# Kernel optimization log

Hardware: AMD Instinct MI355X
Metric: run time of the kernel (lower is better)

The kernel has to match this reference:

```python
import jax, jax.numpy as jnp
import numpy as np

N, E, H, L, B = 200000, 800000, 128, 4, 2000  # nodes, directed edges, hidden, layers, graphs
ATOM, BOND = 28, 6


def setup_inputs() -> dict:
    key = jax.random.key(0)
    ks = jax.random.split(key, 12)
    h = jax.random.normal(ks[0], (N, ATOM), jnp.float32)
    e = jax.random.normal(ks[1], (E, BOND), jnp.float32)
    # paired directed edges: edge 2i = (u->v), edge 2i+1 = (v->u), so rev(k) = k ^ 1
    u = jax.random.randint(ks[2], (E // 2,), 0, N)
    v = jax.random.randint(ks[3], (E // 2,), 0, N)
    src = jnp.stack([u, v], axis=1).reshape(-1)
    dst = jnp.stack([v, u], axis=1).reshape(-1)
    graph_id = jnp.sort(jax.random.randint(ks[4], (N,), 0, B))
    s = 1.0 / np.sqrt(H).astype(np.float32)
    W_emb = jax.random.normal(ks[5], (ATOM, H), jnp.float32) * (1.0 / np.sqrt(ATOM))
    W_init = jax.random.normal(ks[6], (H + BOND, H), jnp.float32) * s
    b_init = jnp.zeros((H,), jnp.float32)
    W_layers = jax.random.normal(ks[7], (L, H, H), jnp.float32) * s
    b_layers = jnp.zeros((L, H), jnp.float32)
    W_ro = jax.random.normal(ks[8], (H, H), jnp.float32) * s
    W_pred = jax.random.normal(ks[9], (H, 1), jnp.float32) * s
    b_pred = jnp.zeros((1,), jnp.float32)
    snorm_n = jnp.ones((N, 1), jnp.float32)
    snorm_e = jnp.ones((E, 1), jnp.float32)
    return dict(h=h, e=e, W_emb=W_emb, W_init=W_init, b_init=b_init,
                W_layers=W_layers, b_layers=b_layers, W_ro=W_ro,
                W_pred=W_pred, b_pred=b_pred, src=src, dst=dst,
                graph_id=graph_id, snorm_n=snorm_n, snorm_e=snorm_e)


def reference(h, e, W_emb, W_init, b_init, W_layers, b_layers, W_ro,
              W_pred, b_pred, src, dst, graph_id, snorm_n, snorm_e):
    n_nodes = h.shape[0]
    n_edges = src.shape[0]
    rev = jnp.arange(n_edges) ^ 1  # paired reverse-edge index
    # node embedding (dropout is identity at p=0); x kept as residual input per source
    x = h @ W_emb  # [N, H]
    # init_message_func: per-edge relu(Linear(cat(h_src, e)))
    he = jax.nn.relu(jnp.concatenate([x[src], e], axis=1) @ W_init + b_init)  # [E, H]
    # D-MPNN layers: aggregate incoming edge states at src node, exclude reverse edge,
    # linear + relu (norms disabled in this config), outer residual add
    n_layers = W_layers.shape[0]
    for l in range(n_layers):
        agg = jax.ops.segment_sum(he, dst, num_segments=n_nodes)  # sum of edge states into each node
        m = agg[src] - he[rev]                                    # exclude reverse edge
        he = jax.nn.relu(m @ W_layers[l] + b_layers[l]) + he      # residual
    # update_all(copy_edge, sum): node state = sum of incoming edge states
    h_out = jax.ops.segment_sum(he, dst, num_segments=n_nodes)  # [N, H]
    h_ro = h_out @ W_ro                                          # linear_ro (no bias)
    # readout == 'sum': per-graph sum of node states
    hg = jax.ops.segment_sum(h_ro, graph_id, num_segments=B)     # [B, H]
    return hg @ W_pred + b_pred                                  # [B, 1]
```

## Files before the change

kernel.cpp:

```cpp
#include <hip/hip_runtime.h>
#include <hip/hip_bf16.h>

#define H 128
#define ATOM 28
#define BOND 6
#define NLAYERS 4
#define TE 32
#define LW 136
#define LKI 72
typedef unsigned short US;
typedef unsigned int UI;
typedef short bf16x8 __attribute__((ext_vector_type(8)));
typedef float f32x4 __attribute__((ext_vector_type(4)));
#define MFMA(a,b,c) __builtin_amdgcn_mfma_f32_16x16x32_bf16((a),(b),(c),0,0,0)

__device__ __forceinline__ float bf2f(US u) {
    union { unsigned int i; float f; } v; v.i = ((unsigned int)u) << 16; return v.f;
}
__device__ __forceinline__ US f2bf(float f) {
    union { float f; unsigned int i; } v; v.f = f;
    unsigned int r = v.i + 0x7FFF + ((v.i >> 16) & 1);
    return (US)(r >> 16);
}
__device__ __forceinline__ float in_ld(const void* p, long long i, int bf) {
    return bf ? bf2f(((const US*)p)[i]) : ((const float*)p)[i];
}

__global__ void detect_kernel(const void* snorm, int* flag) {
    const US* u = (const US*)snorm;
    *flag = (u[0] == 0x3F80 && u[2] == 0x3F80) ? 1 : 0;
}

__global__ void fail_kernel(void* out, int nB, float val, const int* flag) {
    int i = blockIdx.x * 256 + threadIdx.x;
    if (i < nB) {
        if (*flag) ((US*)out)[i] = f2bf(val);
        else       ((float*)out)[i] = val;
    }
}

__global__ void build_wt(const void* __restrict__ W_emb, const void* __restrict__ W_init,
                         const int* __restrict__ flag, US* __restrict__ WtG) {
    int bf = *flag;
    int k = blockIdx.x;
    int c = threadIdx.x;
    float v = 0.f;
    if (k < ATOM) {
        for (int j = 0; j < H; ++j)
            v += in_ld(W_emb, k * H + j, bf) * in_ld(W_init, (long long)j * H + c, bf);
    } else if (k < ATOM + BOND) {
        v = in_ld(W_init, (long long)(H + k - ATOM) * H + c, bf);
    }
    WtG[c * 64 + k] = f2bf(v);
}

__global__ void build_wtL(const void* __restrict__ W_layers, const int* __restrict__ flag,
                          US* __restrict__ WtL) {
    int bf = *flag;
    int l = blockIdx.x >> 7, n = blockIdx.x & 127;
    int k = threadIdx.x;
    long long si = (long long)l * H * H + (long long)k * H + n;
    WtL[((long long)l * H + n) * H + k] = bf ? ((const US*)W_layers)[si]
                                             : f2bf(((const float*)W_layers)[si]);
}

__global__ void build_wtR(const void* __restrict__ W_ro, const int* __restrict__ flag,
                          US* __restrict__ WtR) {
    int bf = *flag;
    int n = blockIdx.x, k = threadIdx.x;
    long long si = (long long)k * H + n;
    WtR[(long long)n * H + k] = bf ? ((const US*)W_ro)[si]
                                   : f2bf(((const float*)W_ro)[si]);
}

__global__ void hist_kernel(const int* __restrict__ dst, int* __restrict__ cnt, int nE) {
    int k = blockIdx.x * 256 + threadIdx.x;
    if (k < nE) atomicAdd(&cnt[dst[k]], 1);
}

__global__ __launch_bounds__(256) void scan1(const int* __restrict__ cnt,
                                             int* __restrict__ rowptr,
                                             int* __restrict__ partials, int nN) {
    __shared__ int sd[256];
    int t = threadIdx.x;
    int base = blockIdx.x * 1024 + t * 4;
    int l0 = (base + 0 < nN) ? cnt[base + 0] : 0;
    int l1 = (base + 1 < nN) ? cnt[base + 1] : 0;
    int l2 = (base + 2 < nN) ? cnt[base + 2] : 0;
    int l3 = (base + 3 < nN) ? cnt[base + 3] : 0;
    int s = l0 + l1 + l2 + l3;
    sd[t] = s; __syncthreads();
    for (int off = 1; off < 256; off <<= 1) {
        int v = (t >= off) ? sd[t - off] : 0;
        __syncthreads();
        sd[t] += v;
        __syncthreads();
    }
    int excl = sd[t] - s;
    if (base + 0 < nN) rowptr[base + 0] = excl;
    if (base + 1 < nN) rowptr[base + 1] = excl + l0;
    if (base + 2 < nN) rowptr[base + 2] = excl + l0 + l1;
    if (base + 3 < nN) rowptr[base + 3] = excl + l0 + l1 + l2;
    if (t == 255) partials[blockIdx.x] = sd[255];
}

__global__ __launch_bounds__(256) void scan2(const int* __restrict__ partials,
                                             int* __restrict__ blockoff, int SB) {
    __shared__ int sd[256];
    int t = threadIdx.x;
    int v = (t < SB) ? partials[t] : 0;
    sd[t] = v; __syncthreads();
    for (int off = 1; off < 256; off <<= 1) {
        int x = (t >= off) ? sd[t - off] : 0;
        __syncthreads();
        sd[t] += x;
        __syncthreads();
    }
    blockoff[t] = sd[t] - v;
}

__global__ void scan3(int* __restrict__ rowptr, int* __restrict__ cursor,
                      const int* __restrict__ blockoff, int nN, int nE) {
    int i = blockIdx.x * 256 + threadIdx.x;
    if (i < nN) {
        int v = rowptr[i] + blockoff[i >> 10];
        rowptr[i] = v;
        cursor[i] = v;
    }
    if (i == 0) rowptr[nN] = nE;
}

__global__ void fill_kernel(const int* __restrict__ dst, int* __restrict__ cursor,
                            int* __restrict__ ein, int nE) {
    int k = blockIdx.x * 256 + threadIdx.x;
    if (k < nE) {
        int pos = atomicAdd(&cursor[dst[k]], 1);
        ein[pos] = k;
    }
}

__global__ __launch_bounds__(256) void agg_gather(
    const US* __restrict__ he, const int* __restrict__ rowptr,
    const int* __restrict__ ein, US* __restrict__ agg, int nN) {
    int n = blockIdx.x * 4 + (threadIdx.x >> 6);
    int lane = threadIdx.x & 63;
    if (n >= nN) return;
    const UI* heU = (const UI*)he;
    int s = rowptr[n], epos = rowptr[n + 1];
    float f0 = 0.f, f1 = 0.f;
    int idx = s;
    for (; idx + 4 <= epos; idx += 4) {
        int e0 = ein[idx], e1 = ein[idx + 1], e2 = ein[idx + 2], e3 = ein[idx + 3];
        UI u0 = heU[(long long)e0 * 64 + lane];
        UI u1 = heU[(long long)e1 * 64 + lane];
        UI u2 = heU[(long long)e2 * 64 + lane];
        UI u3 = heU[(long long)e3 * 64 + lane];
        f0 += bf2f((US)(u0 & 0xFFFF)) + bf2f((US)(u1 & 0xFFFF))
            + bf2f((US)(u2 & 0xFFFF)) + bf2f((US)(u3 & 0xFFFF));
        f1 += bf2f((US)(u0 >> 16)) + bf2f((US)(u1 >> 16))
            + bf2f((US)(u2 >> 16)) + bf2f((US)(u3 >> 16));
    }
    for (; idx < epos; ++idx) {
        UI u = heU[(long long)ein[idx] * 64 + lane];
        f0 += bf2f((US)(u & 0xFFFF));
        f1 += bf2f((US)(u >> 16));
    }
    ((UI*)agg)[(long long)n * 64 + lane] = (UI)f2bf(f0) | ((UI)f2bf(f1) << 16);
}

__global__ __launch_bounds__(256) void scatter_cas(
    const US* __restrict__ he, const int* __restrict__ dst,
    US* __restrict__ agg, long long totalPairs) {
    const UI* heU = (const UI*)he;
    UI* aggU = (UI*)agg;
    long long i = (long long)blockIdx.x * blockDim.x + threadIdx.x;
    long long stride = (long long)gridDim.x * blockDim.x;
    for (; i < totalPairs; i += stride) {
        int k = (int)(i >> 6);
        int jp = (int)(i & 63);
        UI pv = heU[i];
        float v0 = bf2f((US)(pv & 0xFFFF));
        float v1 = bf2f((US)(pv >> 16));
        UI* addr = aggU + (long long)dst[k] * 64 + jp;
        UI old = *addr, assumed;
        do {
            assumed = old;
            UI nv = (UI)f2bf(bf2f((US)(assumed & 0xFFFF)) + v0)
                  | ((UI)f2bf(bf2f((US)(assumed >> 16)) + v1) << 16);
            old = atomicCAS(addr, assumed, nv);
        } while (old != assumed);
    }
}

__global__ __launch_bounds__(256) void mfma_init(
    const void* __restrict__ h, const void* __restrict__ e,
    const US* __restrict__ WtG, const void* __restrict__ b_init,
    const int* __restrict__ src, const int* __restrict__ flag,
    US* __restrict__ he, int nE) {
    __shared__ __align__(16) US sA[TE * LKI];
    const int bf = *flag;
    const int tid = threadIdx.x;
    const int wave = tid >> 6, lane = tid & 63;
    const int quad = lane >> 4, l16 = lane & 15;
    const int ncol0 = wave * 32;
    float rb0 = in_ld(b_init, ncol0 + l16, bf);
    float rb1 = in_ld(b_init, ncol0 + 16 + l16, bf);
    bf16x8 bw[2][2];
    #pragma unroll
    for (int i = 0; i < 2; ++i)
        #pragma unroll
        for (int c = 0; c < 2; ++c)
            bw[i][c] = *(const bf16x8*)&WtG[(ncol0 + c * 16 + l16) * 64 + i * 32 + quad * 8];

    const int r = tid >> 3, u0 = (tid & 7) * 4;
    int ntiles = nE / TE;
    for (int t = blockIdx.x; t < ntiles; t += gridDim.x) {
        int k0 = t * TE;
        __syncthreads();
        {
            int k = k0 + r;
            int s = src[k];
            UI* dU = (UI*)&sA[r * LKI];
            if (bf) {
                const UI* hU = (const UI*)h;
                const UI* eU = (const UI*)e;
                #pragma unroll
                for (int q = 0; q < 4; ++q) {
                    int idx = u0 + q;
                    UI v = 0;
                    if (idx < 14) v = hU[(long long)s * 14 + idx];
                    else if (idx < 17) v = eU[(long long)k * 3 + (idx - 14)];
                    dU[idx] = v;
                }
            } else {
                const float* hF = (const float*)h;
                const float* eF = (const float*)e;
                #pragma unroll
                for (int q = 0; q < 4; ++q) {
                    int idx = u0 + q;
                    int c0 = idx * 2, c1 = idx * 2 + 1;
                    float f0 = 0.f, f1 = 0.f;
                    if (c0 < ATOM) f0 = hF[(long long)s * ATOM + c0];
                    else if (c0 < ATOM + BOND) f0 = eF[(long long)k * BOND + (c0 - ATOM)];
                    if (c1 < ATOM) f1 = hF[(long long)s * ATOM + c1];
                    else if (c1 < ATOM + BOND) f1 = eF[(long long)k * BOND + (c1 - ATOM)];
                    dU[idx] = (UI)f2bf(f0) | ((UI)f2bf(f1) << 16);
                }
            }
        }
        __syncthreads();

        f32x4 acc00 = {0,0,0,0}, acc01 = {0,0,0,0}, acc10 = {0,0,0,0}, acc11 = {0,0,0,0};
        #pragma unroll
        for (int i = 0; i < 2; ++i) {
            int kb = i * 32 + quad * 8;
            bf16x8 a0 = *(const bf16x8*)&sA[l16 * LKI + kb];
            bf16x8 a1 = *(const bf16x8*)&sA[(l16 + 16) * LKI + kb];
            acc00 = MFMA(a0, bw[i][0], acc00);
            acc01 = MFMA(a0, bw[i][1], acc01);
            acc10 = MFMA(a1, bw[i][0], acc10);
            acc11 = MFMA(a1, bw[i][1], acc11);
        }
        #pragma unroll
        for (int mt = 0; mt < 2; ++mt)
            #pragma unroll
            for (int reg = 0; reg < 4; ++reg) {
                int row = mt * 16 + quad * 4 + reg;
                long long hbase = (long long)(k0 + row) * H;
                #pragma unroll
                for (int nt = 0; nt < 2; ++nt) {
                    float a = mt ? (nt ? acc11[reg] : acc10[reg])
                                 : (nt ? acc01[reg] : acc00[reg]);
                    int col = ncol0 + nt * 16 + l16;
                    he[hbase + col] = f2bf(fmaxf(a + (nt ? rb1 : rb0), 0.f));
                }
            }
    }
}

__global__ __launch_bounds__(256) void mfma_layer(
    const US* __restrict__ agg, const int* __restrict__ src,
    const US* __restrict__ WtL, const void* __restrict__ b_layers,
    int layer, const int* __restrict__ flag, US* __restrict__ he, int nE) {
    __shared__ __align__(16) US sHe[TE * LW];
    __shared__ __align__(16) US sAgg[TE * LW];
    const int bf = *flag;
    const int tid = threadIdx.x;
    const int wave = tid >> 6, lane = tid & 63;
    const int quad = lane >> 4, l16 = lane & 15;
    const int ncol0 = wave * 32;
    float rb0 = in_ld(b_layers, (long long)layer * H + ncol0 + l16, bf);
    float rb1 = in_ld(b_layers, (long long)layer * H + ncol0 + 16 + l16, bf);
    const US* Wl = WtL + (size_t)layer * H * H;
    bf16x8 bw[4][2];
    #pragma unroll
    for (int i = 0; i < 4; ++i)
        #pragma unroll
        for (int c = 0; c < 2; ++c)
            bw[i][c] = *(const bf16x8*)&Wl[(ncol0 + c * 16 + l16) * H + i * 32 + quad * 8];

    int ntiles = nE / TE;
    for (int t = blockIdx.x; t < ntiles; t += gridDim.x) {
        int k0 = t * TE;
        __syncthreads();
        const uint4* heG = (const uint4*)(he + (long long)k0 * H);
        #pragma unroll
        for (int ii = 0; ii < 2; ++ii) {
            int i = tid + ii * 256;
            int r = i >> 4, q = i & 15;
            *(uint4*)&sHe[r * LW + q * 8] = heG[i];
            int s = src[k0 + r];
            *(uint4*)&sAgg[r * LW + q * 8] = ((const uint4*)(agg + (long long)s * H))[q];
        }
        __syncthreads();

        f32x4 g1a = {0,0,0,0}, g1b = {0,0,0,0}, g1c = {0,0,0,0}, g1d = {0,0,0,0};
        f32x4 g2a = {0,0,0,0}, g2b = {0,0,0,0}, g2c = {0,0,0,0}, g2d = {0,0,0,0};
        #pragma unroll
        for (int i = 0; i < 4; ++i) {
            int kb = i * 32 + quad * 8;
            bf16x8 aA0 = *(const bf16x8*)&sAgg[l16 * LW + kb];
            bf16x8 aA1 = *(const bf16x8*)&sAgg[(l16 + 16) * LW + kb];
            bf16x8 aH0 = *(const bf16x8*)&sHe[l16 * LW + kb];
            bf16x8 aH1 = *(const bf16x8*)&sHe[(l16 + 16) * LW + kb];
            g1a = MFMA(aA0, bw[i][0], g1a); g1b = MFMA(aA0, bw[i][1], g1b);
            g1c = MFMA(aA1, bw[i][0], g1c); g1d = MFMA(aA1, bw[i][1], g1d);
            g2a = MFMA(aH0, bw[i][0], g2a); g2b = MFMA(aH0, bw[i][1], g2b);
            g2c = MFMA(aH1, bw[i][0], g2c); g2d = MFMA(aH1, bw[i][1], g2d);
        }
        __syncthreads();

        #pragma unroll
        for (int mt = 0; mt < 2; ++mt)
            #pragma unroll
            for (int reg = 0; reg < 4; ++reg) {
                int row = mt * 16 + quad * 4 + reg;
                #pragma unroll
                for (int nt = 0; nt < 2; ++nt) {
                    float g1 = mt ? (nt ? g1d[reg] : g1c[reg])
                                  : (nt ? g1b[reg] : g1a[reg]);
                    float g2 = mt ? (nt ? g2d[reg ^ 1] : g2c[reg ^ 1])
                                  : (nt ? g2b[reg ^ 1] : g2a[reg ^ 1]);
                    int col = ncol0 + nt * 16 + l16;
                    float v = fmaxf(g1 - g2 + (nt ? rb1 : rb0), 0.f)
                            + bf2f(sHe[row * LW + col]);
                    sAgg[row * LW + col] = f2bf(v);
                }
            }
        int row2 = lane >> 1, half = lane & 1;
        int cbase = ncol0 + half * 16;
        uint4 v0 = *(const uint4*)&sAgg[row2 * LW + cbase];
        uint4 v1 = *(const uint4*)&sAgg[row2 * LW + cbase + 8];
        uint4* dst4 = (uint4*)(he + (long long)(k0 + row2) * H + cbase);
        dst4[0] = v0; dst4[1] = v1;
    }
}

__global__ __launch_bounds__(256) void mfma_readout_agg(
    const US* __restrict__ agg, const US* __restrict__ WtR,
    const int* __restrict__ graph_id, float* __restrict__ hg, int nN) {
    __shared__ __align__(16) US sM[TE * LW];
    __shared__ int sGid[TE];
    const int tid = threadIdx.x;
    const int wave = tid >> 6, lane = tid & 63;
    const int quad = lane >> 4, l16 = lane & 15;
    const int ncol0 = wave * 32;
    bf16x8 bw[4][2];
    #pragma unroll
    for (int i = 0; i < 4; ++i)
        #pragma unroll
        for (int c = 0; c < 2; ++c)
            bw[i][c] = *(const bf16x8*)&WtR[(ncol0 + c * 16 + l16) * H + i * 32 + quad * 8];
    const UI* aggU = (const UI*)agg;

    int ntiles = (nN + TE - 1) / TE;
    for (int t = blockIdx.x; t < ntiles; t += gridDim.x) {
        int k0 = t * TE;
        __syncthreads();
        if (tid < TE) sGid[tid] = (k0 + tid < nN) ? graph_id[k0 + tid] : -1;
        for (int i = tid; i < TE * 64; i += 256) {
            int r = i >> 6, c2 = i & 63;
            UI pk = (k0 + r < nN) ? aggU[(long long)(k0 + r) * 64 + c2] : 0u;
            *(UI*)&sM[r * LW + c2 * 2] = pk;
        }
        __syncthreads();
        f32x4 acc00 = {0,0,0,0}, acc01 = {0,0,0,0}, acc10 = {0,0,0,0}, acc11 = {0,0,0,0};
        #pragma unroll
        for (int i = 0; i < 4; ++i) {
            int kb = i * 32 + quad * 8;
            bf16x8 a0 = *(const bf16x8*)&sM[l16 * LW + kb];
            bf16x8 a1 = *(const bf16x8*)&sM[(l16 + 16) * LW + kb];
            acc00 = MFMA(a0, bw[i][0], acc00);
            acc01 = MFMA(a0, bw[i][1], acc01);
            acc10 = MFMA(a1, bw[i][0], acc10);
            acc11 = MFMA(a1, bw[i][1], acc11);
        }
        if (sGid[0] == sGid[TE - 1] && sGid[0] >= 0) {
            long long gb = (long long)sGid[0] * H;
            #pragma unroll
            for (int nt = 0; nt < 2; ++nt) {
                f32x4 s4 = (nt ? acc01 : acc00) + (nt ? acc11 : acc10);
                float v = s4[0] + s4[1] + s4[2] + s4[3];
                v += __shfl_xor(v, 16);
                v += __shfl_xor(v, 32);
                if (quad == 0) unsafeAtomicAdd(&hg[gb + ncol0 + nt * 16 + l16], v);
            }
        } else {
            #pragma unroll
            for (int mt = 0; mt < 2; ++mt)
                #pragma unroll
                for (int reg = 0; reg < 4; ++reg) {
                    int row = mt * 16 + quad * 4 + reg;
                    int gid = sGid[row];
                    if (gid < 0) continue;
                    long long gb = (long long)gid * H;
                    #pragma unroll
                    for (int nt = 0; nt < 2; ++nt) {
                        float a = mt ? (nt ? acc11[reg] : acc10[reg])
                                     : (nt ? acc01[reg] : acc00[reg]);
                        unsafeAtomicAdd(&hg[gb + ncol0 + nt * 16 + l16], a);
                    }
                }
        }
    }
}

__global__ __launch_bounds__(256) void pred_kernel(
    const float* __restrict__ hg, const void* __restrict__ W_pred,
    const void* __restrict__ b_pred, const int* __restrict__ flag,
    void* __restrict__ out, int nB) {
    int bf = *flag;
    int wave = (int)((blockIdx.x * blockDim.x + threadIdx.x) >> 6);
    int lane = threadIdx.x & 63;
    if (wave >= nB) return;
    float v = hg[(long long)wave * H + lane] * in_ld(W_pred, lane, bf) +
              hg[(long long)wave * H + lane + 64] * in_ld(W_pred, lane + 64, bf);
    #pragma unroll
    for (int off = 32; off > 0; off >>= 1) v += __shfl_down(v, off);
    if (lane == 0) {
        float r = v + in_ld(b_pred, 0, bf);
        if (bf) ((US*)out)[wave] = f2bf(r);
        else    ((float*)out)[wave] = r;
    }
}

extern "C" void kernel_launch(void* const* d_in, const int* in_sizes, int n_in,
                              void* d_out, int out_size, void* d_ws, size_t ws_size,
                              hipStream_t stream) {
    const void* h        = d_in[0];
    const void* e        = d_in[1];
    const void* W_emb    = d_in[2];
    const void* W_init   = d_in[3];
    const void* b_init   = d_in[4];
    const void* W_layers = d_in[5];
    const void* b_layers = d_in[6];
    const void* W_ro     = d_in[7];
    const void* W_pred   = d_in[8];
    const void* b_pred   = d_in[9];
    const int*  src      = (const int*)d_in[10];
    const int*  dst      = (const int*)d_in[11];
    const int*  graph_id = (const int*)d_in[12];
    const void* snorm_n  = d_in[13];

    int nN = in_sizes[0] / ATOM;
    int nE = in_sizes[1] / BOND;
    int nB = out_size;
    int SB = (nN + 1023) / 1024;

    size_t off = 0;
    auto alloc = [&](size_t bytes) { size_t o = off; off = (off + bytes + 255) & ~(size_t)255; return o; };
    size_t o_flag = alloc(256);
    size_t o_wt   = alloc((size_t)H * 64 * sizeof(US));
    size_t o_wtL  = alloc((size_t)NLAYERS * H * H * sizeof(US));
    size_t o_wtR  = alloc((size_t)H * H * sizeof(US));
    size_t o_hg   = alloc((size_t)nB * H * sizeof(float));
    size_t o_cnt  = alloc((size_t)nN * sizeof(int));
    size_t o_rp   = alloc((size_t)(nN + 1) * sizeof(int));
    size_t o_cur  = alloc((size_t)nN * sizeof(int));
    size_t o_par  = alloc(256 * sizeof(int));
    size_t o_boff = alloc(256 * sizeof(int));
    size_t o_ein  = alloc((size_t)nE * sizeof(int));
    size_t o_agg  = alloc((size_t)nN * H * sizeof(US));
    size_t o_he   = alloc((size_t)nE * H * sizeof(US));
    size_t needG  = off;

    char* W = (char*)d_ws;
    int*   flag   = (int*)(W + o_flag);
    US*    WtG    = (US*)(W + o_wt);
    US*    WtL    = (US*)(W + o_wtL);
    US*    WtR    = (US*)(W + o_wtR);
    float* hg     = (float*)(W + o_hg);
    int*   cnt    = (int*)(W + o_cnt);
    int*   rowptr = (int*)(W + o_rp);
    int*   cursor = (int*)(W + o_cur);
    int*   part   = (int*)(W + o_par);
    int*   boff   = (int*)(W + o_boff);
    int*   ein    = (int*)(W + o_ein);
    US*    agg    = (US*)(W + o_agg);
    US*    he     = (US*)(W + o_he);

    detect_kernel<<<1, 1, 0, stream>>>(snorm_n, flag);
    build_wt<<<64, 128, 0, stream>>>(W_emb, W_init, flag, WtG);
    build_wtL<<<NLAYERS * H, 128, 0, stream>>>(W_layers, flag, WtL);
    build_wtR<<<H, 128, 0, stream>>>(W_ro, flag, WtR);

    if (ws_size >= needG && SB <= 256) {
        hipMemsetAsync(cnt, 0, (size_t)nN * sizeof(int), stream);
        hist_kernel<<<(nE + 255) / 256, 256, 0, stream>>>(dst, cnt, nE);
        scan1<<<SB, 256, 0, stream>>>(cnt, rowptr, part, nN);
        scan2<<<1, 256, 0, stream>>>(part, boff, SB);
        scan3<<<(nN + 255) / 256, 256, 0, stream>>>(rowptr, cursor, boff, nN, nE);
        fill_kernel<<<(nE + 255) / 256, 256, 0, stream>>>(dst, cursor, ein, nE);

        mfma_init<<<2048, 256, 0, stream>>>(h, e, WtG, b_init, src, flag, he, nE);
        for (int l = 0; l < NLAYERS; ++l) {
            agg_gather<<<(nN + 3) / 4, 256, 0, stream>>>(he, rowptr, ein, agg, nN);
            mfma_layer<<<2048, 256, 0, stream>>>(agg, src, WtL, b_layers, l, flag, he, nE);
        }
        agg_gather<<<(nN + 3) / 4, 256, 0, stream>>>(he, rowptr, ein, agg, nN);
        hipMemsetAsync(hg, 0, (size_t)nB * H * sizeof(float), stream);
        mfma_readout_agg<<<2048, 256, 0, stream>>>(agg, WtR, graph_id, hg, nN);
        pred_kernel<<<(nB + 3) / 4, 256, 0, stream>>>(hg, W_pred, b_pred, flag, d_out, nB);
        return;
    }

    size_t off2 = 0;
    auto alloc2 = [&](size_t bytes) { size_t o = off2; off2 = (off2 + bytes + 255) & ~(size_t)255; return o; };
    alloc2(256);
    alloc2((size_t)H * 64 * sizeof(US));
    alloc2((size_t)NLAYERS * H * H * sizeof(US));
    alloc2((size_t)H * H * sizeof(US));
    size_t f2_hg  = alloc2((size_t)nB * H * sizeof(float));
    size_t f2_agg = alloc2((size_t)nN * H * sizeof(US));
    size_t f2_he  = alloc2((size_t)nE * H * sizeof(US));
    size_t needT  = off2;

    if (ws_size >= needT) {
        float* hg2  = (float*)(W + f2_hg);
        US*    agg2 = (US*)(W + f2_agg);
        US*    he2  = (US*)(W + f2_he);
        mfma_init<<<2048, 256, 0, stream>>>(h, e, WtG, b_init, src, flag, he2, nE);
        for (int l = 0; l < NLAYERS; ++l) {
            hipMemsetAsync(agg2, 0, (size_t)nN * H * sizeof(US), stream);
            scatter_cas<<<2048, 256, 0, stream>>>(he2, dst, agg2, (long long)nE * (H / 2));
            mfma_layer<<<2048, 256, 0, stream>>>(agg2, src, WtL, b_layers, l, flag, he2, nE);
        }
        hipMemsetAsync(agg2, 0, (size_t)nN * H * sizeof(US), stream);
        scatter_cas<<<2048, 256, 0, stream>>>(he2, dst, agg2, (long long)nE * (H / 2));
        hipMemsetAsync(hg2, 0, (size_t)nB * H * sizeof(float), stream);
        mfma_readout_agg<<<2048, 256, 0, stream>>>(agg2, WtR, graph_id, hg2, nN);
        pred_kernel<<<(nB + 3) / 4, 256, 0, stream>>>(hg2, W_pred, b_pred, flag, d_out, nB);
    } else {
        float val = (float)(ws_size >> 20) * 1e6f;
        fail_kernel<<<(nB + 255) / 256, 256, 0, stream>>>(d_out, nB, val, flag);
    }
}
```

Measured before the change: 1.212 ms.

## Fold readout and prediction weights into a vector; double-buffer layer tile loads

Precomputes wp = W_ro @ W_pred so the final readout becomes a per-node dot product fused into the last edge gather. This replaces the final agg_gather, the readout MFMA kernel with B×H atomics, and the pred kernel with a single gather-dot kernel that does scalar per-graph atomics. Separately, mfma_layer now prefetches the next tile's he and agg rows into registers and writes them into double-buffered LDS, so global loads overlap the MFMA work. The cost is twice the shared memory per block and more live registers, and the readout sums in fp32 in a different order than before.

```diff
diff --git a/kernel.cpp b/kernel.cpp
--- a/kernel.cpp
+++ b/kernel.cpp
@@ -64,13 +64,14 @@
                                              : f2bf(((const float*)W_layers)[si]);
 }
 
-__global__ void build_wtR(const void* __restrict__ W_ro, const int* __restrict__ flag,
-                          US* __restrict__ WtR) {
+__global__ void build_wp(const void* __restrict__ W_ro, const void* __restrict__ W_pred,
+                         const int* __restrict__ flag, float* __restrict__ wp) {
     int bf = *flag;
-    int n = blockIdx.x, k = threadIdx.x;
-    long long si = (long long)k * H + n;
-    WtR[(long long)n * H + k] = bf ? ((const US*)W_ro)[si]
-                                   : f2bf(((const float*)W_ro)[si]);
+    int c = threadIdx.x;
+    float s = 0.f;
+    for (int j = 0; j < H; ++j)
+        s += in_ld(W_ro, (long long)c * H + j, bf) * in_ld(W_pred, j, bf);
+    wp[c] = s;
 }
 
 __global__ void hist_kernel(const int* __restrict__ dst, int* __restrict__ cnt, int nE) {
@@ -166,6 +167,107 @@
         f1 += bf2f((US)(u >> 16));
     }
     ((UI*)agg)[(long long)n * 64 + lane] = (UI)f2bf(f0) | ((UI)f2bf(f1) << 16);
+}
+
+__global__ __launch_bounds__(256) void readout_dot(
+    const US* __restrict__ he, const int* __restrict__ rowptr,
+    const int* __restrict__ ein, const float* __restrict__ wp,
+    const int* __restrict__ graph_id, float* __restrict__ hgS, int nN) {
+    __shared__ float sv[4];
+    __shared__ int sg[4];
+    int wave = threadIdx.x >> 6, lane = threadIdx.x & 63;
+    int n = blockIdx.x * 4 + wave;
+    bool valid = n < nN;
+    float w0 = wp[2 * lane], w1 = wp[2 * lane + 1];
+    float v = 0.f;
+    if (valid) {
+        const UI* heU = (const UI*)he;
+        int s = rowptr[n], epos = rowptr[n + 1];
+        float f0 = 0.f, f1 = 0.f;
+        int idx = s;
+        for (; idx + 4 <= epos; idx += 4) {
+            int e0 = ein[idx], e1 = ein[idx + 1], e2 = ein[idx + 2], e3 = ein[idx + 3];
+            UI u0 = heU[(long long)e0 * 64 + lane];
+            UI u1 = heU[(long long)e1 * 64 + lane];
+            UI u2 = heU[(long long)e2 * 64 + lane];
+            UI u3 = heU[(long long)e3 * 64 + lane];
+            f0 += bf2f((US)(u0 & 0xFFFF)) + bf2f((US)(u1 & 0xFFFF))
+                + bf2f((US)(u2 & 0xFFFF)) + bf2f((US)(u3 & 0xFFFF));
+            f1 += bf2f((US)(u0 >> 16)) + bf2f((US)(u1 >> 16))
+                + bf2f((US)(u2 >> 16)) + bf2f((US)(u3 >> 16));
+        }
+        for (; idx < epos; ++idx) {
+            UI u = heU[(long long)ein[idx] * 64 + lane];
+            f0 += bf2f((US)(u & 0xFFFF));
+            f1 += bf2f((US)(u >> 16));
+        }
+        v = f0 * w0 + f1 * w1;
+        #pragma unroll
+        for (int off = 32; off > 0; off >>= 1) v += __shfl_down(v, off);
+    }
+    if (lane == 0) {
+        sv[wave] = valid ? v : 0.f;
+        sg[wave] = valid ? graph_id[n] : -1;
+    }
+    __syncthreads();
+    if (threadIdx.x == 0) {
+        int cg = sg[0]; float acc = sv[0];
+        #pragma unroll
+        for (int w = 1; w < 4; ++w) {
+            if (sg[w] == cg) acc += sv[w];
+            else {
+                if (cg >= 0) unsafeAtomicAdd(&hgS[cg], acc);
+                cg = sg[w]; acc = sv[w];
+            }
+        }
+        if (cg >= 0) unsafeAtomicAdd(&hgS[cg], acc);
+    }
+}
+
+__global__ __launch_bounds__(256) void agg_dot(
+    const US* __restrict__ agg, const float* __restrict__ wp,
+    const int* __restrict__ graph_id, float* __restrict__ hgS, int nN) {
+    __shared__ float sv[4];
+    __shared__ int sg[4];
+    int wave = threadIdx.x >> 6, lane = threadIdx.x & 63;
+    int n = blockIdx.x * 4 + wave;
+    bool valid = n < nN;
+    float v = 0.f;
+    if (valid) {
+        UI u = ((const UI*)agg)[(long long)n * 64 + lane];
+        v = bf2f((US)(u & 0xFFFF)) * wp[2 * lane]
+          + bf2f((US)(u >> 16)) * wp[2 * lane + 1];
+        #pragma unroll
+        for (int off = 32; off > 0; off >>= 1) v += __shfl_down(v, off);
+    }
+    if (lane == 0) {
+        sv[wave] = valid ? v : 0.f;
+        sg[wave] = valid ? graph_id[n] : -1;
+    }
+    __syncthreads();
+    if (threadIdx.x == 0) {
+        int cg = sg[0]; float acc = sv[0];
+        #pragma unroll
+        for (int w = 1; w < 4; ++w) {
+            if (sg[w] == cg) acc += sv[w];
+            else {
+                if (cg >= 0) unsafeAtomicAdd(&hgS[cg], acc);
+                cg = sg[w]; acc = sv[w];
+            }
+        }
+        if (cg >= 0) unsafeAtomicAdd(&hgS[cg], acc);
+    }
+}
+
+__global__ void finish_kernel(const float* __restrict__ hgS, const void* __restrict__ b_pred,
+                              const int* __restrict__ flag, void* __restrict__ out, int nB) {
+    int bf = *flag;
+    int i = blockIdx.x * 256 + threadIdx.x;
+    if (i < nB) {
+        float r = hgS[i] + in_ld(b_pred, 0, bf);
+        if (bf) ((US*)out)[i] = f2bf(r);
+        else    ((float*)out)[i] = r;
+    }
 }
 
 __global__ __launch_bounds__(256) void scatter_cas(
@@ -282,8 +384,8 @@
     const US* __restrict__ agg, const int* __restrict__ src,
     const US* __restrict__ WtL, const void* __restrict__ b_layers,
     int layer, const int* __restrict__ flag, US* __restrict__ he, int nE) {
-    __shared__ __align__(16) US sHe[TE * LW];
-    __shared__ __align__(16) US sAgg[TE * LW];
+    __shared__ __align__(16) US sHe[2][TE * LW];
+    __shared__ __align__(16) US sAgg[2][TE * LW];
     const int bf = *flag;
     const int tid = threadIdx.x;
     const int wave = tid >> 6, lane = tid & 63;
@@ -299,30 +401,45 @@
         for (int c = 0; c < 2; ++c)
             bw[i][c] = *(const bf16x8*)&Wl[(ncol0 + c * 16 + l16) * H + i * 32 + quad * 8];
 
+    const int r0 = tid >> 4, q0 = tid & 15;
     int ntiles = nE / TE;
-    for (int t = blockIdx.x; t < ntiles; t += gridDim.x) {
+    int t = blockIdx.x;
+    uint4 vh0, vh1, va0, va1;
+    if (t < ntiles) {
         int k0 = t * TE;
-        __syncthreads();
         const uint4* heG = (const uint4*)(he + (long long)k0 * H);
-        #pragma unroll
-        for (int ii = 0; ii < 2; ++ii) {
-            int i = tid + ii * 256;
-            int r = i >> 4, q = i & 15;
-            *(uint4*)&sHe[r * LW + q * 8] = heG[i];
-            int s = src[k0 + r];
-            *(uint4*)&sAgg[r * LW + q * 8] = ((const uint4*)(agg + (long long)s * H))[q];
-        }
-        __syncthreads();
+        vh0 = heG[tid]; vh1 = heG[tid + 256];
+        int s0 = src[k0 + r0], s1 = src[k0 + r0 + 16];
+        va0 = ((const uint4*)(agg + (long long)s0 * H))[q0];
+        va1 = ((const uint4*)(agg + (long long)s1 * H))[q0];
+    }
+    int buf = 0;
+    for (; t < ntiles; t += gridDim.x, buf ^= 1) {
+        int k0 = t * TE;
+        *(uint4*)&sHe[buf][r0 * LW + q0 * 8] = vh0;
+        *(uint4*)&sHe[buf][(r0 + 16) * LW + q0 * 8] = vh1;
+        *(uint4*)&sAgg[buf][r0 * LW + q0 * 8] = va0;
+        *(uint4*)&sAgg[buf][(r0 + 16) * LW + q0 * 8] = va1;
+        __syncthreads();
+        int tn = t + gridDim.x;
+        if (tn < ntiles) {
+            int kn = tn * TE;
+            const uint4* heG = (const uint4*)(he + (long long)kn * H);
+            vh0 = heG[tid]; vh1 = heG[tid + 256];
+            int s0 = src[kn + r0], s1 = src[kn + r0 + 16];
+            va0 = ((const uint4*)(agg + (long long)s0 * H))[q0];
+            va1 = ((const uint4*)(agg + (long long)s1 * H))[q0];
+        }
 
         f32x4 g1a = {0,0,0,0}, g1b = {0,0,0,0}, g1c = {0,0,0,0}, g1d = {0,0,0,0};
         f32x4 g2a = {0,0,0,0}, g2b = {0,0,0,0}, g2c = {0,0,0,0}, g2d = {0,0,0,0};
         #pragma unroll
         for (int i = 0; i < 4; ++i) {
             int kb = i * 32 + quad * 8;
-            bf16x8 aA0 = *(const bf16x8*)&sAgg[l16 * LW + kb];
-            bf16x8 aA1 = *(const bf16x8*)&sAgg[(l16 + 16) * LW + kb];
-            bf16x8 aH0 = *(const bf16x8*)&sHe[l16 * LW + kb];
-            bf16x8 aH1 = *(const bf16x8*)&sHe[(l16 + 16) * LW + kb];
+            bf16x8 aA0 = *(const bf16x8*)&sAgg[buf][l16 * LW + kb];
+            bf16x8 aA1 = *(const bf16x8*)&sAgg[buf][(l16 + 16) * LW + kb];
+            bf16x8 aH0 = *(const bf16x8*)&sHe[buf][l16 * LW + kb];
+            bf16x8 aH1 = *(const bf16x8*)&sHe[buf][(l16 + 16) * LW + kb];
             g1a = MFMA(aA0, bw[i][0], g1a); g1b = MFMA(aA0, bw[i][1], g1b);
             g1c = MFMA(aA1, bw[i][0], g1c); g1d = MFMA(aA1, bw[i][1], g1d);
             g2a = MFMA(aH0, bw[i][0], g2a); g2b = MFMA(aH0, bw[i][1], g2b);
@@ -343,104 +460,16 @@
                                   : (nt ? g2b[reg ^ 1] : g2a[reg ^ 1]);
                     int col = ncol0 + nt * 16 + l16;
                     float v = fmaxf(g1 - g2 + (nt ? rb1 : rb0), 0.f)
-                            + bf2f(sHe[row * LW + col]);
-                    sAgg[row * LW + col] = f2bf(v);
+                            + bf2f(sHe[buf][row * LW + col]);
+                    sAgg[buf][row * LW + col] = f2bf(v);
                 }
             }
         int row2 = lane >> 1, half = lane & 1;
         int cbase = ncol0 + half * 16;
-        uint4 v0 = *(const uint4*)&sAgg[row2 * LW + cbase];
-        uint4 v1 = *(const uint4*)&sAgg[row2 * LW + cbase + 8];
+        uint4 o0 = *(const uint4*)&sAgg[buf][row2 * LW + cbase];
+        uint4 o1 = *(const uint4*)&sAgg[buf][row2 * LW + cbase + 8];
         uint4* dst4 = (uint4*)(he + (long long)(k0 + row2) * H + cbase);
-        dst4[0] = v0; dst4[1] = v1;
-    }
-}
-
-__global__ __launch_bounds__(256) void mfma_readout_agg(
-    const US* __restrict__ agg, const US* __restrict__ WtR,
-    const int* __restrict__ graph_id, float* __restrict__ hg, int nN) {
-    __shared__ __align__(16) US sM[TE * LW];
-    __shared__ int sGid[TE];
-    const int tid = threadIdx.x;
-    const int wave = tid >> 6, lane = tid & 63;
-    const int quad = lane >> 4, l16 = lane & 15;
-    const int ncol0 = wave * 32;
-    bf16x8 bw[4][2];
-    #pragma unroll
-    for (int i = 0; i < 4; ++i)
-        #pragma unroll
-        for (int c = 0; c < 2; ++c)
-            bw[i][c] = *(const bf16x8*)&WtR[(ncol0 + c * 16 + l16) * H + i * 32 + quad * 8];
-    const UI* aggU = (const UI*)agg;
-
-    int ntiles = (nN + TE - 1) / TE;
-    for (int t = blockIdx.x; t < ntiles; t += gridDim.x) {
-        int k0 = t * TE;
-        __syncthreads();
-        if (tid < TE) sGid[tid] = (k0 + tid < nN) ? graph_id[k0 + tid] : -1;
-        for (int i = tid; i < TE * 64; i += 256) {
-            int r = i >> 6, c2 = i & 63;
-            UI pk = (k0 + r < nN) ? aggU[(long long)(k0 + r) * 64 + c2] : 0u;
-            *(UI*)&sM[r * LW + c2 * 2] = pk;
-        }
-        __syncthreads();
-        f32x4 acc00 = {0,0,0,0}, acc01 = {0,0,0,0}, acc10 = {0,0,0,0}, acc11 = {0,0,0,0};
-        #pragma unroll
-        for (int i = 0; i < 4; ++i) {
-            int kb = i * 32 + quad * 8;
-            bf16x8 a0 = *(const bf16x8*)&sM[l16 * LW + kb];
-            bf16x8 a1 = *(const bf16x8*)&sM[(l16 + 16) * LW + kb];
-            acc00 = MFMA(a0, bw[i][0], acc00);
-            acc01 = MFMA(a0, bw[i][1], acc01);
-            acc10 = MFMA(a1, bw[i][0], acc10);
-            acc11 = MFMA(a1, bw[i][1], acc11);
-        }
-        if (sGid[0] == sGid[TE - 1] && sGid[0] >= 0) {
-            long long gb = (long long)sGid[0] * H;
-            #pragma unroll
-            for (int nt = 0; nt < 2; ++nt) {
-                f32x4 s4 = (nt ? acc01 : acc00) + (nt ? acc11 : acc10);
-                float v = s4[0] + s4[1] + s4[2] + s4[3];
-                v += __shfl_xor(v, 16);
-                v += __shfl_xor(v, 32);
-                if (quad == 0) unsafeAtomicAdd(&hg[gb + ncol0 + nt * 16 + l16], v);
-            }
-        } else {
-            #pragma unroll
-            for (int mt = 0; mt < 2; ++mt)
-                #pragma unroll
-                for (int reg = 0; reg < 4; ++reg) {
-                    int row = mt * 16 + quad * 4 + reg;
-                    int gid = sGid[row];
-                    if (gid < 0) continue;
-                    long long gb = (long long)gid * H;
-                    #pragma unroll
-                    for (int nt = 0; nt < 2; ++nt) {
-                        float a = mt ? (nt ? acc11[reg] : acc10[reg])
-                                     : (nt ? acc01[reg] : acc00[reg]);
-                        unsafeAtomicAdd(&hg[gb + ncol0 + nt * 16 + l16], a);
-                    }
-                }
-        }
-    }
-}
-
-__global__ __launch_bounds__(256) void pred_kernel(
-    const float* __restrict__ hg, const void* __restrict__ W_pred,
-    const void* __restrict__ b_pred, const int* __restrict__ flag,
-    void* __restrict__ out, int nB) {
-    int bf = *flag;
-    int wave = (int)((blockIdx.x * blockDim.x + threadIdx.x) >> 6);
-    int lane = threadIdx.x & 63;
-    if (wave >= nB) return;
-    float v = hg[(long long)wave * H + lane] * in_ld(W_pred, lane, bf) +
-              hg[(long long)wave * H + lane + 64] * in_ld(W_pred, lane + 64, bf);
-    #pragma unroll
-    for (int off = 32; off > 0; off >>= 1) v += __shfl_down(v, off);
-    if (lane == 0) {
-        float r = v + in_ld(b_pred, 0, bf);
-        if (bf) ((US*)out)[wave] = f2bf(r);
-        else    ((float*)out)[wave] = r;
+        dst4[0] = o0; dst4[1] = o1;
     }
 }
 
@@ -472,8 +501,8 @@
     size_t o_flag = alloc(256);
     size_t o_wt   = alloc((size_t)H * 64 * sizeof(US));
     size_t o_wtL  = alloc((size_t)NLAYERS * H * H * sizeof(US));
-    size_t o_wtR  = alloc((size_t)H * H * sizeof(US));
-    size_t o_hg   = alloc((size_t)nB * H * sizeof(float));
+    size_t o_wp   = alloc((size_t)H * sizeof(float));
+    size_t o_hgs  = alloc((size_t)nB * sizeof(float));
     size_t o_cnt  = alloc((size_t)nN * sizeof(int));
     size_t o_rp   = alloc((size_t)(nN + 1) * sizeof(int));
     size_t o_cur  = alloc((size_t)nN * sizeof(int));
@@ -488,8 +517,8 @@
     int*   flag   = (int*)(W + o_flag);
     US*    WtG    = (US*)(W + o_wt);
     US*    WtL    = (US*)(W + o_wtL);
-    US*    WtR    = (US*)(W + o_wtR);
-    float* hg     = (float*)(W + o_hg);
+    float* wp     = (float*)(W + o_wp);
+    float* hgS    = (float*)(W + o_hgs);
     int*   cnt    = (int*)(W + o_cnt);
     int*   rowptr = (int*)(W + o_rp);
     int*   cursor = (int*)(W + o_cur);
@@ -502,7 +531,7 @@
     detect_kernel<<<1, 1, 0, stream>>>(snorm_n, flag);
     build_wt<<<64, 128, 0, stream>>>(W_emb, W_init, flag, WtG);
     build_wtL<<<NLAYERS * H, 128, 0, stream>>>(W_layers, flag, WtL);
-    build_wtR<<<H, 128, 0, stream>>>(W_ro, flag, WtR);
+    build_wp<<<1, 128, 0, stream>>>(W_ro, W_pred, flag, wp);
 
     if (ws_size >= needG && SB <= 256) {
         hipMemsetAsync(cnt, 0, (size_t)nN * sizeof(int), stream);
@@ -517,10 +546,9 @@
             agg_gather<<<(nN + 3) / 4, 256, 0, stream>>>(he, rowptr, ein, agg, nN);
             mfma_layer<<<2048, 256, 0, stream>>>(agg, src, WtL, b_layers, l, flag, he, nE);
         }
-        agg_gather<<<(nN + 3) / 4, 256, 0, stream>>>(he, rowptr, ein, agg, nN);
-        hipMemsetAsync(hg, 0, (size_t)nB * H * sizeof(float), stream);
-        mfma_readout_agg<<<2048, 256, 0, stream>>>(agg, WtR, graph_id, hg, nN);
-        pred_kernel<<<(nB + 3) / 4, 256, 0, stream>>>(hg, W_pred, b_pred, flag, d_out, nB);
+        hipMemsetAsync(hgS, 0, (size_t)nB * sizeof(float), stream);
+        readout_dot<<<(nN + 3) / 4, 256, 0, stream>>>(he, rowptr, ein, wp, graph_id, hgS, nN);
+        finish_kernel<<<(nB + 255) / 256, 256, 0, stream>>>(hgS, b_pred, flag, d_out, nB);
         return;
     }
 
@@ -529,16 +557,18 @@
     alloc2(256);
     alloc2((size_t)H * 64 * sizeof(US));
     alloc2((size_t)NLAYERS * H * H * sizeof(US));
-    alloc2((size_t)H * H * sizeof(US));
-    size_t f2_hg  = alloc2((size_t)nB * H * sizeof(float));
+    size_t f2_wp  = alloc2((size_t)H * sizeof(float));
+    size_t f2_hgs = alloc2((size_t)nB * sizeof(float));
     size_t f2_agg = alloc2((size_t)nN * H * sizeof(US));
     size_t f2_he  = alloc2((size_t)nE * H * sizeof(US));
     size_t needT  = off2;
 
     if (ws_size >= needT) {
-        float* hg2  = (float*)(W + f2_hg);
+        float* wp2  = (float*)(W + f2_wp);
+        float* hgS2 = (float*)(W + f2_hgs);
         US*    agg2 = (US*)(W + f2_agg);
         US*    he2  = (US*)(W + f2_he);
+        build_wp<<<1, 128, 0, stream>>>(W_ro, W_pred, flag, wp2);
         mfma_init<<<2048, 256, 0, stream>>>(h, e, WtG, b_init, src, flag, he2, nE);
         for (int l = 0; l < NLAYERS; ++l) {
             hipMemsetAsync(agg2, 0, (size_t)nN * H * sizeof(US), stream);
@@ -547,9 +577,9 @@
         }
         hipMemsetAsync(agg2, 0, (size_t)nN * H * sizeof(US), stream);
         scatter_cas<<<2048, 256, 0, stream>>>(he2, dst, agg2, (long long)nE * (H / 2));
-        hipMemsetAsync(hg2, 0, (size_t)nB * H * sizeof(float), stream);
-        mfma_readout_agg<<<2048, 256, 0, stream>>>(agg2, WtR, graph_id, hg2, nN);
-        pred_kernel<<<(nB + 3) / 4, 256, 0, stream>>>(hg2, W_pred, b_pred, flag, d_out, nB);
+        hipMemsetAsync(hgS2, 0, (size_t)nB * sizeof(float), stream);
+        agg_dot<<<(nN + 3) / 4, 256, 0, stream>>>(agg2, wp2, graph_id, hgS2, nN);
+        finish_kernel<<<(nB + 255) / 256, 256, 0, stream>>>(hgS2, b_pred, flag, d_out, nB);
     } else {
         float val = (float)(ws_size >> 20) * 1e6f;
         fail_kernel<<<(nB + 255) / 256, 256, 0, stream>>>(d_out, nB, val, flag);
```

New measurement: 1.112 ms. -8.2%, faster.
